# Performance work log

Hardware: AMD Instinct MI355X
Metric: run time of the kernel (lower is better)

Reference implementation:

```python
import jax, jax.numpy as jnp
import numpy as np
from jax import lax

EPS = 1e-5

def _conv(x, w, pad):
    # x: NCHW, w: OIHW, stride 1
    return lax.conv_general_dilated(x, w, (1, 1), [(pad, pad), (pad, pad)],
                                    dimension_numbers=('NCHW', 'OIHW', 'NCHW'))

def _binconv(x, w):
    # IR-Net/ReActNet HardBinaryConv: sign-binarized weights scaled by per-filter
    # mean |w| (alpha), sign-binarized activations; clip-based STE for backward.
    alpha = jnp.mean(jnp.abs(w), axis=(1, 2, 3), keepdims=True)  # [O,1,1,1]
    wc = jnp.clip(w, -1.0, 1.0)
    bw = lax.stop_gradient(alpha * jnp.sign(w) - wc) + wc
    xc = jnp.clip(x, -1.0, 1.0)
    ba = lax.stop_gradient(jnp.sign(x) - xc) + xc
    return _conv(ba, bw, 1)

def _bn(x, g, b, m, v):
    # inference-mode BatchNorm2d with running stats
    inv = g / jnp.sqrt(v + EPS)
    return x * inv[None, :, None, None] + (b - m * inv)[None, :, None, None]

def _pool(x):
    return lax.reduce_window(x, -jnp.inf, lax.max, (1, 1, 2, 2), (1, 1, 2, 2), 'VALID')

def _htanh(x):
    return jnp.clip(x, -1.0, 1.0)

def setup_inputs() -> dict:
    key = jax.random.key(0)
    ks = jax.random.split(key, 40)
    B = 256
    d = {'x': jax.random.normal(ks[0], (B, 3, 32, 32), jnp.float32)}
    shapes = [(128, 3, 3, 3), (128, 128, 3, 3), (256, 128, 3, 3),
              (256, 256, 3, 3), (512, 256, 3, 3), (512, 512, 3, 3)]
    chans = [128, 128, 256, 256, 512, 512]
    ki = 1
    for i, (ws, c) in enumerate(zip(shapes, chans)):
        fan_in = ws[1] * 9
        d[f'w{i}'] = jax.random.normal(ks[ki], ws, jnp.float32) / np.sqrt(fan_in); ki += 1
        d[f'g{i}'] = jnp.ones((c,), jnp.float32)
        d[f'b{i}'] = jnp.zeros((c,), jnp.float32)
        d[f'm{i}'] = jax.random.normal(ks[ki], (c,), jnp.float32) * 0.1; ki += 1
        d[f'v{i}'] = jax.random.uniform(ks[ki], (c,), jnp.float32, 0.5, 1.5); ki += 1
    d['fcw'] = jax.random.normal(ks[ki], (10, 512 * 4 * 4), jnp.float32) * 0.01
    d['fcb'] = jnp.zeros((10,), jnp.float32)
    return d

def reference(x, w0, g0, b0, m0, v0, w1, g1, b1, m1, v1, w2, g2, b2, m2, v2,
              w3, g3, b3, m3, v3, w4, g4, b4, m4, v4, w5, g5, b5, m5, v5,
              fcw, fcb):
    h = _bn(_conv(x, w0, 1), g0, b0, m0, v0)            # [B,128,32,32]
    h = _htanh(_bn(_pool(_binconv(h, w1)), g1, b1, m1, v1))   # [B,128,16,16]
    h = _htanh(_bn(_binconv(h, w2), g2, b2, m2, v2))          # [B,256,16,16]
    h = _htanh(_bn(_pool(_binconv(h, w3)), g3, b3, m3, v3))   # [B,256,8,8]
    h = _htanh(_bn(_binconv(h, w4), g4, b4, m4, v4))          # [B,512,8,8]
    h = _htanh(_bn(_pool(_binconv(h, w5)), g5, b5, m5, v5))   # [B,512,4,4]
    h = h.reshape(h.shape[0], -1)                             # [B,8192]
    return h @ fcw.T + fcb                                    # [B,10]
```

## Files before the change

kernel.cpp:

```cpp
#include <hip/hip_runtime.h>
#include <cstdint>

#define EPS 1e-5
typedef unsigned long long u64;
typedef unsigned int u32;

struct BnArgs { const float *g[6], *b[6], *m[6], *v[6]; };
struct PackArgs { const float* w[5]; u64* wbt[5]; };

__global__ void bn_prep_all(BnArgs p, double* __restrict__ scale_all,
                            double* __restrict__ shift_all) {
    int i = blockIdx.x * 256 + threadIdx.x;
    if (i >= 1792) return;
    int l, base;
    if (i < 128)       { l = 0; base = 0; }
    else if (i < 256)  { l = 1; base = 128; }
    else if (i < 512)  { l = 2; base = 256; }
    else if (i < 768)  { l = 3; base = 512; }
    else if (i < 1280) { l = 4; base = 768; }
    else               { l = 5; base = 1280; }
    const int c = i - base;
    double inv = (double)p.g[l][c] / sqrt((double)p.v[l][c] + EPS);
    scale_all[i] = inv;
    shift_all[i] = (double)p.b[l][c] - (double)p.m[l][c] * inv;
}

__global__ void zero_out(float* __restrict__ out, int n) {
    int i = blockIdx.x * blockDim.x + threadIdx.x;
    if (i < n) out[i] = 0.f;
}

__global__ void zero_u64(u64* __restrict__ p, size_t n) {
    size_t i = (size_t)blockIdx.x * 256 + threadIdx.x;
    const size_t step = (size_t)gridDim.x * 256;
    for (; i < n; i += step) p[i] = 0ull;
}

__global__ void pack_all(PackArgs pk, const double* __restrict__ scale_all,
                         double* __restrict__ A_all, u32* __restrict__ ct_all) {
    const int ob = blockIdx.x;
    const int t = threadIdx.x;
    int l, base, Cin, bnoff, OTOT, ctoff;
    if (ob < 128)       { l = 0; base = 0;    Cin = 128; bnoff = 128;  OTOT = 128; ctoff = 0; }
    else if (ob < 384)  { l = 1; base = 128;  Cin = 128; bnoff = 256;  OTOT = 256; ctoff = 2048; }
    else if (ob < 640)  { l = 2; base = 384;  Cin = 256; bnoff = 512;  OTOT = 256; ctoff = 6144; }
    else if (ob < 1152) { l = 3; base = 640;  Cin = 256; bnoff = 768;  OTOT = 512; ctoff = 10240; }
    else                { l = 4; base = 1152; Cin = 512; bnoff = 1280; OTOT = 512; ctoff = 18432; }
    const int o = ob - base;
    const float* wo = pk.w[l] + (size_t)o * Cin * 9;

    double s = 0.0;
    for (int k = t; k < Cin * 9; k += 256) s += fabs((double)wo[k]);
    __shared__ double red[256];
    __shared__ u32 stp[9];
    red[t] = s;
    if (t < 9) stp[t] = 0;
    __syncthreads();
    for (int r = 128; r > 0; r >>= 1) {
        if (t < r) red[t] += red[t + r];
        __syncthreads();
    }
    if (t == 0) {
        double alpha = red[0] / (double)(Cin * 9);
        A_all[ob] = alpha * scale_all[bnoff + o];
    }

    const int W64 = Cin / 64;
    u64* wbt = pk.wbt[l];
    for (int e = t; e < 9 * W64; e += 256) {
        int tap = e / W64, word = e % W64;
        u64 bits = 0;
        for (int j = 0; j < 64; ++j) {
            int c = word * 64 + j;
            if (wo[c * 9 + tap] < 0.f) bits |= (1ull << j);
        }
        wbt[((size_t)tap * OTOT + o) * W64 + word] = bits;
        atomicAdd(&stp[tap], (u32)__popcll(bits));
    }
    __syncthreads();

    if (t < 16) {
        const int pat = t;
        int nv = 0;
        u32 cor = 0;
#pragma unroll
        for (int tap = 0; tap < 9; ++tap) {
            const int dy = tap / 3, dx = tap % 3;
            const bool inv = ((pat & 1) && dy == 0) || ((pat & 2) && dy == 2) ||
                             ((pat & 4) && dx == 0) || ((pat & 8) && dx == 2);
            if (inv) cor += stp[tap]; else nv++;
        }
        ct_all[ctoff + pat * OTOT + o] = (u32)(nv * 64 * W64) + 2u * cor;
    }
}

__global__ __launch_bounds__(256) void conv0_pack(
        const float* __restrict__ x, const float* __restrict__ w0,
        const double* __restrict__ scale, const double* __restrict__ shift,
        u64* __restrict__ bits0) {
    __shared__ double wlds[128 * 27];
    __shared__ double sc[128], sh[128];
    const int tid = threadIdx.x;
    for (int e = tid; e < 128 * 27; e += 256) wlds[e] = (double)w0[e];
    for (int e = tid; e < 128; e += 256) { sc[e] = scale[e]; sh[e] = shift[e]; }
    __syncthreads();

    const int n = blockIdx.y;
    const int p = blockIdx.x * 256 + tid;
    const int y = p >> 5, xx = p & 31;
    const float* xn = x + (size_t)n * 3 * 32 * 32;

    double win[27];
#pragma unroll
    for (int c = 0; c < 3; ++c)
#pragma unroll
        for (int dy = 0; dy < 3; ++dy)
#pragma unroll
            for (int dx = 0; dx < 3; ++dx) {
                const int yy = y + dy - 1, xs = xx + dx - 1;
                const bool ok = (yy >= 0 && yy < 32 && xs >= 0 && xs < 32);
                win[(c * 3 + dy) * 3 + dx] = ok ? (double)xn[(c * 32 + yy) * 32 + xs] : 0.0;
            }

    u64* op = bits0 + (((size_t)n * 34 + (y + 1)) * 34 + (xx + 1)) * 2;
#pragma unroll
    for (int og = 0; og < 2; ++og) {
        u64 word = 0;
#pragma unroll 2
        for (int j = 0; j < 64; ++j) {
            const int o = og * 64 + j;
            const double* wo = &wlds[o * 27];
            double acc = 0.0;
#pragma unroll
            for (int k = 0; k < 27; ++k) acc = fma(wo[k], win[k], acc);
            const double val = acc * sc[o] + sh[o];
            word |= (u64)(val < 0.0) << j;
        }
        op[og] = word;
    }
}

template<int H, int W, int W64, int OTOT, bool POOL, bool LAST, int MINW>
__global__ __launch_bounds__(256, MINW) void bconv6(
        const u64* __restrict__ in_bits, const u64* __restrict__ wbt,
        const double* __restrict__ A, const double* __restrict__ B,
        const u32* __restrict__ ct_all, int ctoff,
        u32* __restrict__ out_bits, float* __restrict__ h5) {
    const int tid = threadIdx.x;
    const int wave = tid >> 6, lane = tid & 63;
    constexpr int OPW = 32;
    constexpr int WPI = (H * W) / 64;
    constexpr int IPB = (WPI >= 4) ? 1 : (4 / WPI);
    const int img = (IPB == 1) ? blockIdx.z : blockIdx.z * IPB + wave;
    const int wii = (IPB == 1) ? (blockIdx.y * 4 + wave) : 0;
    const int y = wii * (64 / W) + lane / W;
    const int x = lane % W;
    const int obase = blockIdx.x * OPW;

    __shared__ u64 wl[9 * OPW * W64];
    __shared__ u32 ctl[16 * 33];
    __shared__ double Ald[OPW], Bld[OPW];
    {
        for (int e = tid; e < 9 * OPW * W64; e += 256) {
            const int tap = e / (OPW * W64), r = e % (OPW * W64);
            wl[e] = wbt[((size_t)tap * OTOT + obase) * W64 + r];
        }
        for (int e = tid; e < 16 * OPW; e += 256) {
            const int pat = e >> 5, oc = e & 31;
            ctl[pat * 33 + oc] = ct_all[ctoff + pat * OTOT + obase + oc];
        }
        for (int e = tid; e < OPW; e += 256) {
            Ald[e] = A[obase + e];
            Bld[e] = B[obase + e];
        }
    }
    __syncthreads();

    constexpr int RC = W + 2;
    const u64* ib = in_bits + (size_t)img * (H + 2) * RC * W64;

    int acc[OPW];
#pragma unroll
    for (int i = 0; i < OPW; ++i) acc[i] = 0;

#pragma unroll 1
    for (int dy = 0; dy < 3; ++dy) {
#pragma unroll 1
        for (int dx = 0; dx < 3; ++dx) {
            const u64* q = ib + ((size_t)(y + dy) * RC + (x + dx)) * W64;
            u64 wn[W64];
#pragma unroll
            for (int k = 0; k < W64; ++k) wn[k] = q[k];
            const u64* wt = &wl[(dy * 3 + dx) * OPW * W64];
#pragma unroll
            for (int oc = 0; oc < OPW; ++oc) {
#pragma unroll
                for (int k = 0; k < W64; ++k)
                    acc[oc] += (int)__popcll(wn[k] ^ wt[oc * W64 + k]);
            }
        }
    }

    const int pat = (y == 0 ? 1 : 0) | (y == H - 1 ? 2 : 0) |
                    (x == 0 ? 4 : 0) | (x == W - 1 ? 8 : 0);
    const int ctbase = pat * 33;
    constexpr int Hp = POOL ? H / 2 : H, Wp = POOL ? W / 2 : W;
    const bool writer = (!POOL) || (((lane & 1) == 0) && ((lane & W) == 0));
    const int py = POOL ? (y >> 1) : y, px = POOL ? (x >> 1) : x;

    u32 cur = 0;
#pragma unroll
    for (int oc = 0; oc < OPW; ++oc) {
        int v = (int)ctl[ctbase + oc] - 2 * acc[oc];
        if (POOL) {
            int v2 = max(v, __shfl_xor(v, 1, 64));
            v = max(v2, __shfl_xor(v2, W, 64));
        }
        const double t = fma(Ald[oc], (double)v, Bld[oc]);
        if (LAST) {
            const double hcl = fmin(1.0, fmax(-1.0, t));
            if (writer)
                h5[(((size_t)img * OTOT + obase + oc) * Hp + py) * Wp + px] = (float)hcl;
        } else {
            cur |= (u32)(t < 0.0) << oc;
        }
    }
    if (!LAST && writer) {
        out_bits[(((size_t)img * (Hp + 2) + (py + 1)) * (Wp + 2) + (px + 1)) * (OTOT / 32)
                 + (obase >> 5)] = cur;
    }
}

__global__ void fc_kernel(const float* __restrict__ h, const float* __restrict__ fcw,
                          const float* __restrict__ fcb, float* __restrict__ out) {
    const int n = blockIdx.x, t = threadIdx.x;
    double acc[10];
#pragma unroll
    for (int j = 0; j < 10; ++j) acc[j] = 0.0;
    const float* hn = h + (size_t)n * 8192;
    for (int k = t; k < 8192; k += 256) {
        double xv = (double)hn[k];
#pragma unroll
        for (int j = 0; j < 10; ++j) acc[j] += xv * (double)fcw[j * 8192 + k];
    }
    __shared__ double red[10][256];
#pragma unroll
    for (int j = 0; j < 10; ++j) red[j][t] = acc[j];
    __syncthreads();
    for (int r = 128; r > 0; r >>= 1) {
        if (t < r) {
#pragma unroll
            for (int j = 0; j < 10; ++j) red[j][t] += red[j][t + r];
        }
        __syncthreads();
    }
    if (t < 10) out[n * 10 + t] = (float)(red[t][0] + (double)fcb[t]);
}

extern "C" void kernel_launch(void* const* d_in, const int* in_sizes, int n_in,
                              void* d_out, int out_size, void* d_ws, size_t ws_size,
                              hipStream_t stream) {
    const float* X = (const float*)d_in[0];
    BnArgs bn;
    PackArgs pk;
    const float* Wt0 = (const float*)d_in[1];
    for (int i = 0; i < 6; ++i) {
        bn.g[i] = (const float*)d_in[2 + 5 * i];
        bn.b[i] = (const float*)d_in[3 + 5 * i];
        bn.m[i] = (const float*)d_in[4 + 5 * i];
        bn.v[i] = (const float*)d_in[5 + 5 * i];
    }
    for (int i = 0; i < 5; ++i) pk.w[i] = (const float*)d_in[1 + 5 * (i + 1)];
    const float* fcw = (const float*)d_in[31];
    const float* fcb = (const float*)d_in[32];
    float* out = (float*)d_out;

    char* ws = (char*)d_ws;
    size_t off = 0;
    auto alloc = [&](size_t bytes) -> void* {
        void* p = ws + off;
        off = (off + bytes + 255) & ~(size_t)255;
        return p;
    };

    double* scale_all = (double*)alloc(1792 * sizeof(double));
    double* shift_all = (double*)alloc(1792 * sizeof(double));
    double* A_all     = (double*)alloc(1664 * sizeof(double));
    u32* ct_all       = (u32*)alloc(26624 * sizeof(u32));
    const size_t WBN[5] = {128ull * 9 * 2, 256ull * 9 * 2, 256ull * 9 * 4,
                           512ull * 9 * 4, 512ull * 9 * 8};
    for (int i = 0; i < 5; ++i) pk.wbt[i] = (u64*)alloc(WBN[i] * sizeof(u64));
    u64* bits4 = (u64*)alloc(256ull * 10 * 10 * 8 * sizeof(u64));
    u64* bits0 = (u64*)alloc(256ull * 34 * 34 * 2 * sizeof(u64));
    u64* bits1 = (u64*)alloc(256ull * 18 * 18 * 2 * sizeof(u64));
    u64* bits2 = (u64*)alloc(256ull * 18 * 18 * 4 * sizeof(u64));
    u64* bits3 = (u64*)alloc(256ull * 10 * 10 * 4 * sizeof(u64));
    const size_t bits_u64 =
        256ull * (10 * 10 * 8 + 34 * 34 * 2 + 18 * 18 * 2 + 18 * 18 * 4 + 10 * 10 * 4);
    float* h5 = (float*)bits0;
    {
        const size_t h5_bytes = 256ull * 8192 * sizeof(float);
        const size_t have = (size_t)((char*)(bits3 + 256ull * 10 * 10 * 4) - (char*)bits0);
        if (h5_bytes > have) alloc(h5_bytes - have);
    }

    if (off > ws_size) {
        zero_out<<<dim3((out_size + 255) / 256), dim3(256), 0, stream>>>(out, out_size);
        return;
    }

    const int BOF[6] = {0, 128, 256, 512, 768, 1280};
    const int AOF[5] = {0, 128, 384, 640, 1152};
    const int CTO[5] = {0, 2048, 6144, 10240, 18432};

    bn_prep_all<<<dim3(7), dim3(256), 0, stream>>>(bn, scale_all, shift_all);
    pack_all<<<dim3(1664), dim3(256), 0, stream>>>(pk, scale_all, A_all, ct_all);
    zero_u64<<<dim3(2048), dim3(256), 0, stream>>>(bits4, bits_u64);

    conv0_pack<<<dim3(4, 256), dim3(256), 0, stream>>>(
        X, Wt0, scale_all + BOF[0], shift_all + BOF[0], bits0);

    bconv6<32, 32, 2, 128, true, false, 4><<<dim3(4, 4, 256), dim3(256), 0, stream>>>(
        bits0, pk.wbt[0], A_all + AOF[0], shift_all + BOF[1], ct_all, CTO[0],
        (u32*)bits1, nullptr);
    bconv6<16, 16, 2, 256, false, false, 4><<<dim3(8, 1, 256), dim3(256), 0, stream>>>(
        bits1, pk.wbt[1], A_all + AOF[1], shift_all + BOF[2], ct_all, CTO[1],
        (u32*)bits2, nullptr);
    bconv6<16, 16, 4, 256, true, false, 4><<<dim3(8, 1, 256), dim3(256), 0, stream>>>(
        bits2, pk.wbt[2], A_all + AOF[2], shift_all + BOF[3], ct_all, CTO[2],
        (u32*)bits3, nullptr);
    bconv6<8, 8, 4, 512, false, false, 4><<<dim3(16, 1, 64), dim3(256), 0, stream>>>(
        bits3, pk.wbt[3], A_all + AOF[3], shift_all + BOF[4], ct_all, CTO[3],
        (u32*)bits4, nullptr);
    bconv6<8, 8, 8, 512, true, true, 4><<<dim3(16, 1, 64), dim3(256), 0, stream>>>(
        bits4, pk.wbt[4], A_all + AOF[4], shift_all + BOF[5], ct_all, CTO[4],
        nullptr, h5);

    fc_kernel<<<dim3(256), dim3(256), 0, stream>>>(h5, fcw, fcb, out);
}
```

Before: 586.8 us.

## Read binary conv weights directly from global memory and halve output channels per block in deep layers

Removes the shared-memory staging of packed weights and BN scale/shift, so every thread reads the weight words straight from global memory, where they are wave-uniform and cached. The last two binary conv layers now compute 16 output channels per block instead of 32, with twice as many blocks and a higher occupancy hint, and write 16-bit halves of the packed output words. This targets the block-prologue load cost and low occupancy in the small-spatial layers, but adds global loads inside the popcount loop and sub-word stores that two blocks make to the same 32-bit word.

```diff
diff --git a/kernel.cpp b/kernel.cpp
--- a/kernel.cpp
+++ b/kernel.cpp
@@ -4,6 +4,7 @@
 #define EPS 1e-5
 typedef unsigned long long u64;
 typedef unsigned int u32;
+typedef unsigned short u16;
 
 struct BnArgs { const float *g[6], *b[6], *m[6], *v[6]; };
 struct PackArgs { const float* w[5]; u64* wbt[5]; };
@@ -140,39 +141,25 @@
     }
 }
 
-template<int H, int W, int W64, int OTOT, bool POOL, bool LAST, int MINW>
-__global__ __launch_bounds__(256, MINW) void bconv6(
+template<int H, int W, int W64, int OTOT, int OPW, bool POOL, bool LAST, int MINW>
+__global__ __launch_bounds__(256, MINW) void bconv7(
         const u64* __restrict__ in_bits, const u64* __restrict__ wbt,
         const double* __restrict__ A, const double* __restrict__ B,
         const u32* __restrict__ ct_all, int ctoff,
         u32* __restrict__ out_bits, float* __restrict__ h5) {
     const int tid = threadIdx.x;
     const int wave = tid >> 6, lane = tid & 63;
-    constexpr int OPW = 32;
     constexpr int WPI = (H * W) / 64;
-    constexpr int IPB = (WPI >= 4) ? 1 : (4 / WPI);
-    const int img = (IPB == 1) ? blockIdx.z : blockIdx.z * IPB + wave;
-    const int wii = (IPB == 1) ? (blockIdx.y * 4 + wave) : 0;
+    const int img = (WPI >= 4) ? blockIdx.z : (blockIdx.z * 4 + wave);
+    const int wii = (WPI >= 4) ? (blockIdx.y * 4 + wave) : 0;
     const int y = wii * (64 / W) + lane / W;
     const int x = lane % W;
     const int obase = blockIdx.x * OPW;
 
-    __shared__ u64 wl[9 * OPW * W64];
-    __shared__ u32 ctl[16 * 33];
-    __shared__ double Ald[OPW], Bld[OPW];
-    {
-        for (int e = tid; e < 9 * OPW * W64; e += 256) {
-            const int tap = e / (OPW * W64), r = e % (OPW * W64);
-            wl[e] = wbt[((size_t)tap * OTOT + obase) * W64 + r];
-        }
-        for (int e = tid; e < 16 * OPW; e += 256) {
-            const int pat = e >> 5, oc = e & 31;
-            ctl[pat * 33 + oc] = ct_all[ctoff + pat * OTOT + obase + oc];
-        }
-        for (int e = tid; e < OPW; e += 256) {
-            Ald[e] = A[obase + e];
-            Bld[e] = B[obase + e];
-        }
+    __shared__ u32 ctl[16 * (OPW + 1)];
+    for (int e = tid; e < 16 * OPW; e += 256) {
+        const int pat = e / OPW, oc = e % OPW;
+        ctl[pat * (OPW + 1) + oc] = ct_all[ctoff + pat * OTOT + obase + oc];
     }
     __syncthreads();
 
@@ -181,7 +168,7 @@
 
     int acc[OPW];
 #pragma unroll
-    for (int i = 0; i < OPW; ++i) acc[i] = 0;
+    for (int oc = 0; oc < OPW; ++oc) acc[oc] = 0;
 
 #pragma unroll 1
     for (int dy = 0; dy < 3; ++dy) {
@@ -191,7 +178,7 @@
             u64 wn[W64];
 #pragma unroll
             for (int k = 0; k < W64; ++k) wn[k] = q[k];
-            const u64* wt = &wl[(dy * 3 + dx) * OPW * W64];
+            const u64* wt = wbt + (size_t)((dy * 3 + dx) * OTOT + obase) * W64;
 #pragma unroll
             for (int oc = 0; oc < OPW; ++oc) {
 #pragma unroll
@@ -203,7 +190,7 @@
 
     const int pat = (y == 0 ? 1 : 0) | (y == H - 1 ? 2 : 0) |
                     (x == 0 ? 4 : 0) | (x == W - 1 ? 8 : 0);
-    const int ctbase = pat * 33;
+    const int ctbase = pat * (OPW + 1);
     constexpr int Hp = POOL ? H / 2 : H, Wp = POOL ? W / 2 : W;
     const bool writer = (!POOL) || (((lane & 1) == 0) && ((lane & W) == 0));
     const int py = POOL ? (y >> 1) : y, px = POOL ? (x >> 1) : x;
@@ -216,7 +203,7 @@
             int v2 = max(v, __shfl_xor(v, 1, 64));
             v = max(v2, __shfl_xor(v2, W, 64));
         }
-        const double t = fma(Ald[oc], (double)v, Bld[oc]);
+        const double t = fma(A[obase + oc], (double)v, B[obase + oc]);
         if (LAST) {
             const double hcl = fmin(1.0, fmax(-1.0, t));
             if (writer)
@@ -226,8 +213,15 @@
         }
     }
     if (!LAST && writer) {
-        out_bits[(((size_t)img * (Hp + 2) + (py + 1)) * (Wp + 2) + (px + 1)) * (OTOT / 32)
-                 + (obase >> 5)] = cur;
+        const size_t wordIdx =
+            (((size_t)img * (Hp + 2) + (py + 1)) * (Wp + 2) + (px + 1)) * (OTOT / 32)
+            + (obase >> 5);
+        if (OPW == 32) {
+            out_bits[wordIdx] = cur;
+        } else {
+            u16* o16 = (u16*)out_bits;
+            o16[wordIdx * 2 + ((obase >> 4) & 1)] = (u16)cur;
+        }
     }
 }
 
@@ -320,19 +314,19 @@
     conv0_pack<<<dim3(4, 256), dim3(256), 0, stream>>>(
         X, Wt0, scale_all + BOF[0], shift_all + BOF[0], bits0);
 
-    bconv6<32, 32, 2, 128, true, false, 4><<<dim3(4, 4, 256), dim3(256), 0, stream>>>(
+    bconv7<32, 32, 2, 128, 32, true, false, 4><<<dim3(4, 4, 256), dim3(256), 0, stream>>>(
         bits0, pk.wbt[0], A_all + AOF[0], shift_all + BOF[1], ct_all, CTO[0],
         (u32*)bits1, nullptr);
-    bconv6<16, 16, 2, 256, false, false, 4><<<dim3(8, 1, 256), dim3(256), 0, stream>>>(
+    bconv7<16, 16, 2, 256, 32, false, false, 4><<<dim3(8, 1, 256), dim3(256), 0, stream>>>(
         bits1, pk.wbt[1], A_all + AOF[1], shift_all + BOF[2], ct_all, CTO[1],
         (u32*)bits2, nullptr);
-    bconv6<16, 16, 4, 256, true, false, 4><<<dim3(8, 1, 256), dim3(256), 0, stream>>>(
+    bconv7<16, 16, 4, 256, 32, true, false, 4><<<dim3(8, 1, 256), dim3(256), 0, stream>>>(
         bits2, pk.wbt[2], A_all + AOF[2], shift_all + BOF[3], ct_all, CTO[2],
         (u32*)bits3, nullptr);
-    bconv6<8, 8, 4, 512, false, false, 4><<<dim3(16, 1, 64), dim3(256), 0, stream>>>(
+    bconv7<8, 8, 4, 512, 16, false, false, 8><<<dim3(32, 1, 64), dim3(256), 0, stream>>>(
         bits3, pk.wbt[3], A_all + AOF[3], shift_all + BOF[4], ct_all, CTO[3],
         (u32*)bits4, nullptr);
-    bconv6<8, 8, 8, 512, true, true, 4><<<dim3(16, 1, 64), dim3(256), 0, stream>>>(
+    bconv7<8, 8, 8, 512, 16, true, true, 8><<<dim3(32, 1, 64), dim3(256), 0, stream>>>(
         bits4, pk.wbt[4], A_all + AOF[4], shift_all + BOF[5], ct_all, CTO[4],
         nullptr, h5);
 
```

Result: faster. 559.6 us, median of 2 (-4.6%).
